# Performance work log

Measured on AMD Instinct MI355X. Metric: run time of the kernel, lower is better.

## Reference

```python
import jax, jax.numpy as jnp
from jax import lax
import numpy as np


def _conv(x, w, b):
    y = lax.conv_general_dilated(x, w, (1, 1), 'VALID', dimension_numbers=('NCHW', 'OIHW', 'NCHW'))
    return y + b[None, :, None, None]


def _prelu(x, a):
    return jnp.where(x > 0, x, a[None, :, None, None] * x)


def _pnet(x, c1w, c1b, p1, c2w, c2b, p2, c3w, c3b, p3, w41, b41, w42, b42):
    x = _prelu(_conv(x, c1w, c1b), p1)
    H, W = x.shape[2], x.shape[3]
    # MaxPool2d(2,2, ceil_mode=True): pad bottom/right with -inf when odd
    x = lax.reduce_window(x, -jnp.inf, lax.max, (1, 1, 2, 2), (1, 1, 2, 2),
                          ((0, 0), (0, 0), (0, H % 2), (0, W % 2)))
    x = _prelu(_conv(x, c2w, c2b), p2)
    x = _prelu(_conv(x, c3w, c3b), p3)
    a = jax.nn.softmax(_conv(x, w41, b41), axis=1)
    b = _conv(x, w42, b42)
    return b, a


def _nms(boxes, scores, imgidx, valid, thr):
    # masked, fixed-size batched NMS (per-image via coordinate offset trick)
    N = boxes.shape[0]
    order = jnp.argsort(-jnp.where(valid, scores, -1e9))
    b = boxes[order] + imgidx[order].astype(boxes.dtype)[:, None] * 1e5
    v = valid[order]
    x1, y1, x2, y2 = b[:, 0], b[:, 1], b[:, 2], b[:, 3]
    area = jnp.maximum(x2 - x1, 0.0) * jnp.maximum(y2 - y1, 0.0)
    ar = jnp.arange(N)

    def body(i, keep):
        iw = jnp.maximum(jnp.minimum(x2[i], x2) - jnp.maximum(x1[i], x1), 0.0)
        ih = jnp.maximum(jnp.minimum(y2[i], y2) - jnp.maximum(y1[i], y1), 0.0)
        inter = iw * ih
        iou = inter / (area[i] + area - inter + 1e-9)
        return keep & ~((iou > thr) & (ar > i) & keep[i])

    keep = lax.fori_loop(0, N, body, v)
    return order, keep


def _detect(images, c1w, c1b, p1, c2w, c2b, p2, c3w, c3b, p3, w41, b41, w42, b42):
    params = (c1w, c1b, p1, c2w, c2b, p2, c3w, c3b, p3, w41, b41, w42, b42)
    x = jnp.transpose(images, (0, 3, 1, 2))  # NHWC -> NCHW
    B, _, H, W = x.shape
    m = 12.0 / 20.0  # 12 / minsize
    scales = []
    ml, si = min(H, W) * m, m
    while ml >= 12:
        scales.append(si)
        si *= 0.709
        ml *= 0.709
    KS, THR0 = 512, 0.6  # fixed per-scale candidate capacity
    all_b, all_i, all_k = [], [], []
    for scale in scales:
        nh, nw = int(H * scale + 1), int(W * scale + 1)
        im = jax.image.resize(x, (B, 3, nh, nw), method='linear')
        im = (im - 127.5) * 0.0078125
        reg, label = _pnet(im, *params)
        probs = label[:, 1]  # [B,h,w]
        b_, h_, w_ = probs.shape
        yy, xx = jnp.meshgrid(jnp.arange(h_), jnp.arange(w_), indexing='ij')
        bbx = jnp.tile(xx.reshape(-1), b_).astype(x.dtype)
        bby = jnp.tile(yy.reshape(-1), b_).astype(x.dtype)
        # stride=2, cellsize=12 grid-cell -> image-space boxes
        q = [jnp.floor((2 * bbx + 1) / scale), jnp.floor((2 * bby + 1) / scale),
             jnp.floor((2 * bbx + 12) / scale), jnp.floor((2 * bby + 12) / scale)]
        score = probs.reshape(-1)
        reg4 = jnp.transpose(reg, (0, 2, 3, 1)).reshape(-1, 4)
        boxes9 = jnp.concatenate([jnp.stack(q + [score], axis=1), reg4], axis=1)  # [N,9]
        imgidx = jnp.repeat(jnp.arange(b_), h_ * w_)
        k = min(KS, boxes9.shape[0])
        vals, idx = lax.top_k(jnp.where(score >= THR0, score, -1e9), k)
        bsel, isel, vsel = boxes9[idx], imgidx[idx], vals > -1e8
        order, keep = _nms(bsel[:, :4], bsel[:, 4], isel, vsel, 0.5)
        all_b.append(bsel[order])
        all_i.append(isel[order])
        all_k.append(keep)
    boxes = jnp.concatenate(all_b, 0)
    iidx = jnp.concatenate(all_i, 0)
    kp = jnp.concatenate(all_k, 0)
    K2 = min(1024, boxes.shape[0])
    vals, idx = lax.top_k(jnp.where(kp, boxes[:, 4], -1e9), K2)
    b2, i2, v2 = boxes[idx], iidx[idx], vals > -1e8
    order, keep = _nms(b2[:, :4], b2[:, 4], i2, v2, 0.7)
    b2 = b2[order]
    regw, regh = b2[:, 2] - b2[:, 0], b2[:, 3] - b2[:, 1]
    out = jnp.stack([b2[:, 0] + b2[:, 5] * regw, b2[:, 1] + b2[:, 6] * regh,
                     b2[:, 2] + b2[:, 7] * regw, b2[:, 3] + b2[:, 8] * regh, b2[:, 4]], axis=1)
    # rerec: square-ify
    hh, ww = out[:, 3] - out[:, 1], out[:, 2] - out[:, 0]
    l = jnp.maximum(hh, ww)
    x1 = out[:, 0] + ww * 0.5 - l * 0.5
    y1 = out[:, 1] + hh * 0.5 - l * 0.5
    out = jnp.stack([x1, y1, x1 + l, y1 + l, out[:, 4]], axis=1)
    return out * keep[:, None].astype(out.dtype)  # invalid/suppressed rows zeroed


def setup_inputs():
    key = jax.random.key(0)
    ks = jax.random.split(key, 16)
    rn = lambda k, s, sc=0.1: jax.random.normal(k, s, dtype=jnp.float32) * sc
    return {
        'images': jax.random.uniform(ks[0], (8, 768, 768, 3), dtype=jnp.float32) * 255.0,
        'c1w': rn(ks[1], (10, 3, 3, 3)), 'c1b': rn(ks[2], (10,)),
        'p1': 0.25 * jnp.ones((10,), jnp.float32),
        'c2w': rn(ks[3], (16, 10, 3, 3)), 'c2b': rn(ks[4], (16,)),
        'p2': 0.25 * jnp.ones((16,), jnp.float32),
        'c3w': rn(ks[5], (32, 16, 3, 3)), 'c3b': rn(ks[6], (32,)),
        'p3': 0.25 * jnp.ones((32,), jnp.float32),
        'w41': rn(ks[7], (2, 32, 1, 1)), 'b41': rn(ks[8], (2,)),
        'w42': rn(ks[9], (4, 32, 1, 1)), 'b42': rn(ks[10], (4,)),
    }


def reference(images, c1w, c1b, p1, c2w, c2b, p2, c3w, c3b, p3, w41, b41, w42, b42):
    return _detect(images, c1w, c1b, p1, c2w, c2b, p2, c3w, c3b, p3, w41, b41, w42, b42)
```

## Files before the change

### kernel.cpp

```cpp
#include <hip/hip_runtime.h>
#include <stdint.h>

typedef unsigned long long u64;
typedef unsigned int u32;

#define TPB 256
#define NJMAX 12
#define NSC 11

__device__ __forceinline__ int findJob(const int* cum, int nj, int v) {
  int j = 0;
  while (j + 1 < nj && v >= cum[j + 1]) ++j;
  return j;
}

struct MkP { int ns; int nw[NSC]; float invs[NSC], ks[NSC];
             int oxB[NSC], T[NSC], wOff[NSC]; };

__global__ void k_mkweights(int* __restrict__ tX0, int* __restrict__ tCNT,
                            float* __restrict__ tWT, float* __restrict__ tW, MkP P) {
  const int s = blockIdx.x;
  const int nw = P.nw[s];
  const float invs = P.invs[s], ks = P.ks[s];
  const int T = P.T[s];
  for (int ox = threadIdx.x; ox < nw; ox += TPB) {
    float sx = ((float)ox + 0.5f) * invs - 0.5f;
    int x0 = (int)ceilf(sx - ks); if (x0 < 0) x0 = 0;
    int x1 = (int)floorf(sx + ks); if (x1 > 767) x1 = 767;
    float wt = 0.f;
    float* wv = tW + P.wOff[s];
    for (int j = x0; j <= x1; ++j) {
      float w = fmaxf(0.f, 1.f - fabsf(sx - (float)j) / ks);
      wt += w;
      wv[(j - x0) * nw + ox] = w;
    }
    for (int k = x1 - x0 + 1; k < T; ++k) wv[k * nw + ox] = 0.f;
    int g = P.oxB[s] + ox;
    tX0[g] = x0; tCNT[g] = x1 - x0 + 1; tWT[g] = wt;
  }
}

struct DscP { int nj; int N[NJMAX]; int hOff[NJMAX], imgOff[NJMAX];
              int oxB[NJMAX], wOff[NJMAX];
              int cumW[NJMAX + 1], cumR[NJMAX + 1]; };

__global__ void k_mkdesc(int* __restrict__ hd, int* __restrict__ vd,
                         int hdcap, int vdcap, DscP P) {
  int gid = blockIdx.x * TPB + threadIdx.x;
  int totW = P.cumW[P.nj], totR = P.cumR[P.nj];
  if (gid < totW) {
    int j = findJob(P.cumW, P.nj, gid);
    int local = gid - P.cumW[j];
    int N = P.N[j];
    int ox = local % N, c = local / N;
    hd[gid]             = P.hOff[j] + c * 768 * N + ox;
    hd[hdcap + gid]     = c * 769;
    hd[2 * hdcap + gid] = N;
    hd[3 * hdcap + gid] = P.oxB[j] + ox;
    hd[4 * hdcap + gid] = P.wOff[j] + ox;
  }
  if (gid < totR) {
    int j = findJob(P.cumR, P.nj, gid);
    int local = gid - P.cumR[j];
    int N = P.N[j];
    int oy = local % N, q = local / N;
    vd[gid]             = P.hOff[j] + q * 768 * N;
    vd[vdcap + gid]     = P.imgOff[j] + (q * N + oy) * N;
    vd[2 * vdcap + gid] = P.oxB[j] + oy;
    vd[3 * vdcap + gid] = P.wOff[j] + oy;
    vd[4 * vdcap + gid] = N;
  }
}

__global__ void k_resizeH_d(const float* __restrict__ img, float* __restrict__ base,
                            const int* __restrict__ tX0, const int* __restrict__ tCNT,
                            const float* __restrict__ tWT, const float* __restrict__ tW,
                            const int* __restrict__ hd, int hdcap, int total) {
  __shared__ float row[3][769];
  const int y = blockIdx.x, b = blockIdx.y;
  const float* src = img + ((long)b * 768 + y) * 768 * 3;
  for (int t = threadIdx.x; t < 2304; t += TPB) {
    int x = t / 3, c = t - 3 * x;
    row[c][x] = src[t];
  }
  __syncthreads();
  const float* rowF = &row[0][0];
  const long yb = (long)y + 2304L * b;
  for (int t = threadIdx.x; t < total; t += TPB) {
    int A = hd[t];
    int R = hd[hdcap + t];
    int N = hd[2 * hdcap + t];
    int g = hd[3 * hdcap + t];
    int W = hd[4 * hdcap + t];
    int x0 = tX0[g], cnt = tCNT[g];
    float wt = tWT[g];
    const float* wv = tW + W;
    const float* rp = rowF + R + x0;
    float acc = 0.f;
    int k = 0;
    for (; k + 3 < cnt; k += 4) {
      float v0 = rp[k],     w0 = wv[(long)k * N];
      float v1 = rp[k + 1], w1 = wv[(long)(k + 1) * N];
      float v2 = rp[k + 2], w2 = wv[(long)(k + 2) * N];
      float v3 = rp[k + 3], w3 = wv[(long)(k + 3) * N];
      acc += v0 * w0; acc += v1 * w1; acc += v2 * w2; acc += v3 * w3;
    }
    for (; k < cnt; ++k) acc += rp[k] * wv[(long)k * N];
    base[(long)A + (long)N * yb] = acc / wt;
  }
}

__global__ void k_resizeV_row(const float* __restrict__ basep, float* __restrict__ img,
                              const int* __restrict__ tX0, const int* __restrict__ tCNT,
                              const float* __restrict__ tWT, const float* __restrict__ tW,
                              const int* __restrict__ vd, int vdcap, int nRows) {
  int row = blockIdx.x * 4 + (threadIdx.x >> 6);
  if (row >= nRows) return;
  int lane = threadIdx.x & 63;
  int S = vd[row];
  int O = vd[vdcap + row];
  int g = vd[2 * vdcap + row];
  int W = vd[3 * vdcap + row];
  int N = vd[4 * vdcap + row];
  int y0 = tX0[g], cnt = tCNT[g];
  float wt = tWT[g];
  const float* wv = tW + W;
  const float* col0 = basep + S + (long)y0 * N;
  for (int ox = lane; ox < N; ox += 64) {
    const float* col = col0 + ox;
    float acc = 0.f;
    int k = 0;
    for (; k + 3 < cnt; k += 4) {
      float v0 = col[(long)k * N],       w0 = wv[(long)k * N];
      float v1 = col[(long)(k + 1) * N], w1 = wv[(long)(k + 1) * N];
      float v2 = col[(long)(k + 2) * N], w2 = wv[(long)(k + 2) * N];
      float v3 = col[(long)(k + 3) * N], w3 = wv[(long)(k + 3) * N];
      acc += v0 * w0; acc += v1 * w1; acc += v2 * w2; acc += v3 * w3;
    }
    for (; k < cnt; ++k) acc += col[(long)k * N] * wv[(long)k * N];
    img[(long)O + ox] = (acc / wt - 127.5f) * 0.0078125f;
  }
}

__device__ __forceinline__ void conv1pool_body(
    const float* in, const float* w, const float* bias, const float* pr,
    float* out, int H, int W, int co, int b, int px, int py) {
  const int h1 = H - 2, w1 = W - 2;
  const int PH = (h1 + 1) >> 1, PW = (w1 + 1) >> 1;
  if (px >= PW || py >= PH) return;
  const int x0 = px * 2, y0 = py * 2;
  float a00 = 0.f, a01 = 0.f, a10 = 0.f, a11 = 0.f;
  const float* wp = w + (long)co * 27;
  const long HW = (long)H * W;
  const float* pp = in + ((long)b * 3 * H + y0) * W + x0;
  for (int ci = 0; ci < 3; ++ci, pp += HW) {
    const float* r = pp;
    float r00 = r[0], r01 = r[1], r02 = r[2], r03 = r[3]; r += W;
    float r10 = r[0], r11 = r[1], r12 = r[2], r13 = r[3]; r += W;
    float r20 = r[0], r21 = r[1], r22 = r[2], r23 = r[3]; r += W;
    float r30 = r[0], r31 = r[1], r32 = r[2], r33 = r[3];
    const float* wc = wp + ci * 9;
    float w0 = wc[0], w1_ = wc[1], w2 = wc[2];
    float w3 = wc[3], w4 = wc[4], w5 = wc[5];
    float w6 = wc[6], w7 = wc[7], w8 = wc[8];
    a00 += r00 * w0 + r01 * w1_ + r02 * w2;
    a00 += r10 * w3 + r11 * w4 + r12 * w5;
    a00 += r20 * w6 + r21 * w7 + r22 * w8;
    a01 += r01 * w0 + r02 * w1_ + r03 * w2;
    a01 += r11 * w3 + r12 * w4 + r13 * w5;
    a01 += r21 * w6 + r22 * w7 + r23 * w8;
    a10 += r10 * w0 + r11 * w1_ + r12 * w2;
    a10 += r20 * w3 + r21 * w4 + r22 * w5;
    a10 += r30 * w6 + r31 * w7 + r32 * w8;
    a11 += r11 * w0 + r12 * w1_ + r13 * w2;
    a11 += r21 * w3 + r22 * w4 + r23 * w5;
    a11 += r31 * w6 + r32 * w7 + r33 * w8;
  }
  const float bb = bias[co], al = pr[co];
  const bool vx = (x0 + 1 < w1), vy = (y0 + 1 < h1);
  float v = a00 + bb; v = v > 0.f ? v : al * v;
  float m = v;
  if (vx) { v = a01 + bb; v = v > 0.f ? v : al * v; m = fmaxf(m, v); }
  if (vy) { v = a10 + bb; v = v > 0.f ? v : al * v; m = fmaxf(m, v); }
  if (vx && vy) { v = a11 + bb; v = v > 0.f ? v : al * v; m = fmaxf(m, v); }
  out[(((long)b * 10 + co) * PH + py) * PW + px] = m;
}

struct C1P { int nj; int nh[NJMAX]; int imgOff[NJMAX], poolOff[NJMAX];
             int t1x[NJMAX]; int cumT[NJMAX + 1]; };

__global__ void k_conv1pool_job(const float* __restrict__ imgb, const float* __restrict__ w,
                                const float* __restrict__ bias, const float* __restrict__ pr,
                                float* __restrict__ poolb, C1P P) {
  int j = findJob(P.cumT, P.nj, blockIdx.x);
  int local = blockIdx.x - P.cumT[j];
  int t1x = P.t1x[j];
  int tX = local % t1x, tY = local / t1x;
  conv1pool_body(imgb + P.imgOff[j], w, bias, pr, poolb + P.poolOff[j],
                 P.nh[j], P.nh[j], blockIdx.y, blockIdx.z,
                 tX * 16 + (threadIdx.x & 15), tY * 16 + (threadIdx.x >> 4));
}

__device__ __forceinline__ void conv3x3c8_body(
    const float* in, const float* w, const float* bias, const float* pr,
    float* out, int Cin, int Cout, int H, int W, int cog, int b, int x0, int y) {
  const int OH = H - 2, OW = W - 2;
  if (y >= OH || x0 >= OW) return;
  float acc[8][4];
#pragma unroll
  for (int k = 0; k < 8; ++k) { acc[k][0] = 0.f; acc[k][1] = 0.f; acc[k][2] = 0.f; acc[k][3] = 0.f; }
  const float* wp = w + (long)cog * Cin * 9;
  const long HW = (long)H * W;
  const float* pp = in + ((long)b * Cin * H + y) * W + x0;
  for (int ci = 0; ci < Cin; ++ci, pp += HW) {
    const float* r = pp;
    float q00 = r[0], q01 = r[1], q02 = r[2], q03 = r[3], q04 = r[4], q05 = r[5]; r += W;
    float q10 = r[0], q11 = r[1], q12 = r[2], q13 = r[3], q14 = r[4], q15 = r[5]; r += W;
    float q20 = r[0], q21 = r[1], q22 = r[2], q23 = r[3], q24 = r[4], q25 = r[5];
#pragma unroll
    for (int k = 0; k < 8; ++k) {
      const float* wc = wp + ((long)k * Cin + ci) * 9;
      float w0 = wc[0], w1 = wc[1], w2 = wc[2];
      float w3 = wc[3], w4 = wc[4], w5 = wc[5];
      float w6 = wc[6], w7 = wc[7], w8 = wc[8];
      acc[k][0] += q00 * w0 + q01 * w1 + q02 * w2;
      acc[k][1] += q01 * w0 + q02 * w1 + q03 * w2;
      acc[k][2] += q02 * w0 + q03 * w1 + q04 * w2;
      acc[k][3] += q03 * w0 + q04 * w1 + q05 * w2;
      acc[k][0] += q10 * w3 + q11 * w4 + q12 * w5;
      acc[k][1] += q11 * w3 + q12 * w4 + q13 * w5;
      acc[k][2] += q12 * w3 + q13 * w4 + q14 * w5;
      acc[k][3] += q13 * w3 + q14 * w4 + q15 * w5;
      acc[k][0] += q20 * w6 + q21 * w7 + q22 * w8;
      acc[k][1] += q21 * w6 + q22 * w7 + q23 * w8;
      acc[k][2] += q22 * w6 + q23 * w7 + q24 * w8;
      acc[k][3] += q23 * w6 + q24 * w7 + q25 * w8;
    }
  }
  const int rem = OW - x0;
#pragma unroll
  for (int k = 0; k < 8; ++k) {
    const int co = cog + k;
    const float bb = bias[co], al = pr[co];
    float* op = out + (((long)b * Cout + co) * OH + y) * OW + x0;
    float v0 = acc[k][0] + bb; v0 = v0 > 0.f ? v0 : al * v0;
    op[0] = v0;
    if (rem > 1) { float v = acc[k][1] + bb; v = v > 0.f ? v : al * v; op[1] = v; }
    if (rem > 2) { float v = acc[k][2] + bb; v = v > 0.f ? v : al * v; op[2] = v; }
    if (rem > 3) { float v = acc[k][3] + bb; v = v > 0.f ? v : al * v; op[3] = v; }
  }
}

struct CvP { int nj; int H[NJMAX]; int inOff[NJMAX], outOff[NJMAX];
             int tx[NJMAX]; int cumT[NJMAX + 1]; };

__global__ void k_conv3x3c8_job(const float* __restrict__ inb, const float* __restrict__ w,
                                const float* __restrict__ bias, const float* __restrict__ pr,
                                float* __restrict__ outb, int Cin, int Cout, CvP P) {
  int j = findJob(P.cumT, P.nj, blockIdx.x);
  int local = blockIdx.x - P.cumT[j];
  int tx0 = P.tx[j];
  int tX = local % tx0, tY = local / tx0;
  conv3x3c8_body(inb + P.inOff[j], w, bias, pr, outb + P.outOff[j], Cin, Cout,
                 P.H[j], P.H[j], blockIdx.y * 8, blockIdx.z,
                 tX * 64 + (threadIdx.x & 15) * 4, tY * 16 + (threadIdx.x >> 4));
}

__device__ __forceinline__ void head_body(const float* x3, const float* w41,
                                          const float* b41, const float* w42,
                                          const float* b42, float* reg, u64* keys,
                                          int plane, long idx) {
  int b = (int)(idx / plane); int rem = (int)(idx % plane);
  const float* p = x3 + (long)b * 32 * plane + rem;
  float l0 = 0.f, l1 = 0.f, r0 = 0.f, r1 = 0.f, r2 = 0.f, r3 = 0.f;
  for (int c = 0; c < 32; ++c) {
    float v = p[(long)c * plane];
    l0 += v * w41[c];      l1 += v * w41[32 + c];
    r0 += v * w42[c];      r1 += v * w42[32 + c];
    r2 += v * w42[64 + c]; r3 += v * w42[96 + c];
  }
  l0 += b41[0]; l1 += b41[1];
  r0 += b42[0]; r1 += b42[1]; r2 += b42[2]; r3 += b42[3];
  float mx = fmaxf(l0, l1);
  float e0 = expf(l0 - mx), e1 = expf(l1 - mx);
  float s = e1 / (e0 + e1);
  reg[idx * 4 + 0] = r0; reg[idx * 4 + 1] = r1;
  reg[idx * 4 + 2] = r2; reg[idx * 4 + 3] = r3;
  u32 ic = 0xFFFFFFFFu - (u32)idx;
  u64 k = (s >= 0.6f) ? ((((u64)__float_as_uint(s)) << 32) | ic) : (u64)ic;
  keys[idx] = k;
}

struct HdP { int nj; int h3[NJMAX]; int c3Off[NJMAX], kOff[NJMAX];
             int cumC[NJMAX + 1]; };

__global__ void k_head_job(const float* __restrict__ c3b, const float* __restrict__ w41,
                           const float* __restrict__ b41, const float* __restrict__ w42,
                           const float* __restrict__ b42, float* __restrict__ regb,
                           u64* __restrict__ keysb, HdP P) {
  int gid = blockIdx.x * TPB + threadIdx.x;
  if (gid >= P.cumC[P.nj]) return;
  int j = findJob(P.cumC, P.nj, gid);
  int idx = gid - P.cumC[j];
  head_body(c3b + P.c3Off[j], w41, b41, w42, b42,
            regb + 4L * P.kOff[j], keysb + P.kOff[j], P.h3[j] * P.h3[j], idx);
}

__device__ __forceinline__ void bitonic2048(u64* s) {
  for (int k = 2; k <= 2048; k <<= 1) {
    for (int j = k >> 1; j > 0; j >>= 1) {
      for (int i = threadIdx.x; i < 2048; i += TPB) {
        int ixj = i ^ j;
        if (ixj > i) {
          u64 a = s[i], b = s[ixj];
          bool desc = ((i & k) == 0);
          if (desc ? (a < b) : (a > b)) { s[i] = b; s[ixj] = a; }
        }
      }
      __syncthreads();
    }
  }
}

__global__ void k_topk(const u64* __restrict__ in, int n, u64* __restrict__ out, int K) {
  __shared__ u64 s[2048];
  int base = blockIdx.x * 2048;
  for (int t = threadIdx.x; t < 2048; t += TPB) {
    int gi = base + t;
    s[t] = (gi < n) ? in[gi] : 0ULL;
  }
  __syncthreads();
  bitonic2048(s);
  for (int t = threadIdx.x; t < K; t += TPB)
    out[(long)blockIdx.x * K + t] = s[t];
}

struct TkP { int nj; int srcSel[NJMAX]; int srcOff[NJMAX]; int n[NJMAX];
             int dstOff[NJMAX]; int cumB[NJMAX + 1]; };

__global__ void k_topk_job(u64* __restrict__ A, u64* __restrict__ B, TkP P) {
  __shared__ u64 s[2048];
  int j = findJob(P.cumB, P.nj, blockIdx.x);
  int lb = blockIdx.x - P.cumB[j];
  const u64* src = (P.srcSel[j] ? B : A) + P.srcOff[j];
  u64* dst = (P.srcSel[j] ? A : B) + P.dstOff[j];
  int n = P.n[j];
  int base = lb * 2048;
  for (int t = threadIdx.x; t < 2048; t += TPB) {
    int gi = base + t;
    s[t] = (gi < n) ? src[gi] : 0ULL;
  }
  __syncthreads();
  bitonic2048(s);
  for (int t = threadIdx.x; t < 512; t += TPB)
    dst[(long)lb * 512 + t] = s[t];
}

struct TkFP { int nj; int srcSel[NJMAX]; int srcOff[NJMAX]; int n[NJMAX]; int sIdx[NJMAX]; };

__global__ void k_topk_fin(const u64* __restrict__ A, const u64* __restrict__ B,
                           u64* __restrict__ selk, TkFP P) {
  __shared__ u64 s[2048];
  int j = blockIdx.x;
  const u64* src = (P.srcSel[j] ? B : A) + P.srcOff[j];
  int n = P.n[j];
  for (int t = threadIdx.x; t < 2048; t += TPB)
    s[t] = (t < n) ? src[t] : 0ULL;
  __syncthreads();
  bitonic2048(s);
  for (int t = threadIdx.x; t < 512; t += TPB)
    selk[(long)P.sIdx[j] * 512 + t] = s[t];
}

__device__ __forceinline__ void gather_body(const u64* keys, const float* reg,
                                            float* boxes, int h, int w, float scalef,
                                            int i) {
  float* bx = boxes + (long)i * 12;
  u64 key = keys[i];
  if ((key >> 32) == 0ULL) {
    for (int q = 0; q < 12; ++q) bx[q] = 0.f;
    return;
  }
  u32 cell = 0xFFFFFFFFu - (u32)(key & 0xFFFFFFFFu);
  int x = (int)(cell % (u32)w); u32 t2 = cell / (u32)w;
  int y = (int)(t2 % (u32)h); int b = (int)(t2 / (u32)h);
  float fx = (float)x, fy = (float)y;
  bx[0] = floorf((2.f * fx + 1.f) / scalef);
  bx[1] = floorf((2.f * fy + 1.f) / scalef);
  bx[2] = floorf((2.f * fx + 12.f) / scalef);
  bx[3] = floorf((2.f * fy + 12.f) / scalef);
  bx[4] = __uint_as_float((u32)(key >> 32));
  bx[5] = reg[(long)cell * 4 + 0];
  bx[6] = reg[(long)cell * 4 + 1];
  bx[7] = reg[(long)cell * 4 + 2];
  bx[8] = reg[(long)cell * 4 + 3];
  bx[9] = (float)b;
  bx[10] = 1.f;
  bx[11] = 0.f;
}

struct GtP { int nj; int h3[NJMAX]; float scalef[NJMAX]; int kOff[NJMAX]; int sIdx[NJMAX]; };

__global__ void k_gather_job(const u64* __restrict__ selk, const float* __restrict__ regb,
                             float* __restrict__ boxes, GtP P) {
  int j = blockIdx.x >> 1;
  int i = ((blockIdx.x & 1) << 8) + threadIdx.x;
  gather_body(selk + (long)P.sIdx[j] * 512, regb + 4L * P.kOff[j],
              boxes + (long)P.sIdx[j] * 512 * 12, P.h3[j], P.h3[j], P.scalef[j], i);
}

__global__ void k_nms(float* __restrict__ boxes, int per, float thr) {
  __shared__ float sx1[1024], sy1[1024], sx2[1024], sy2[1024], sar[1024];
  __shared__ unsigned char kp[1024];
  __shared__ int snv;
  float* bs = boxes + (long)blockIdx.x * per * 12;
  int N = per;
  if (threadIdx.x == 0) snv = 0;
  __syncthreads();
  for (int i = threadIdx.x; i < N; i += blockDim.x) {
    const float* b = bs + (long)i * 12;
    float off = b[9] * 100000.0f;
    float a0 = b[0] + off, a1 = b[1] + off, a2 = b[2] + off, a3 = b[3] + off;
    sx1[i] = a0; sy1[i] = a1; sx2[i] = a2; sy2[i] = a3;
    sar[i] = fmaxf(a2 - a0, 0.f) * fmaxf(a3 - a1, 0.f);
    bool v = (b[10] != 0.f);
    kp[i] = v;
    if (v) atomicMax(&snv, i + 1);
  }
  __syncthreads();
  int nv = snv;
  for (int i = 0; i < nv; ++i) {
    if (kp[i]) {
      float xi1 = sx1[i], yi1 = sy1[i], xi2 = sx2[i], yi2 = sy2[i], ai = sar[i];
      for (int j = threadIdx.x; j < nv; j += blockDim.x) {
        if (j > i && kp[j]) {
          float iw = fmaxf(fminf(xi2, sx2[j]) - fmaxf(xi1, sx1[j]), 0.f);
          float ih = fmaxf(fminf(yi2, sy2[j]) - fmaxf(yi1, sy1[j]), 0.f);
          float inter = iw * ih;
          float iou = inter / (ai + sar[j] - inter + 1e-9f);
          if (iou > thr) kp[j] = 0;
        }
      }
    }
    __syncthreads();
  }
  for (int i = threadIdx.x; i < N; i += blockDim.x)
    bs[(long)i * 12 + 11] = kp[i] ? 1.f : 0.f;
}

__global__ void k_finalkeys(const float* __restrict__ boxes, u64* __restrict__ keys,
                            int total, int padded) {
  int i = blockIdx.x * blockDim.x + threadIdx.x;
  if (i >= padded) return;
  u64 k = 0ULL;
  if (i < total) {
    const float* b = boxes + (long)i * 12;
    u32 ic = 0xFFFFFFFFu - (u32)i;
    k = (b[11] != 0.f) ? ((((u64)__float_as_uint(b[4])) << 32) | ic) : (u64)ic;
  }
  keys[i] = k;
}

__global__ void k_gatherfinal(const u64* __restrict__ keys, const float* __restrict__ boxes,
                              float* __restrict__ sel) {
  int i = blockIdx.x * blockDim.x + threadIdx.x;
  if (i >= 1024) return;
  u64 key = keys[i];
  float* o = sel + (long)i * 12;
  if ((key >> 32) == 0ULL) {
    for (int q = 0; q < 12; ++q) o[q] = 0.f;
    return;
  }
  u32 bi = 0xFFFFFFFFu - (u32)(key & 0xFFFFFFFFu);
  const float* b = boxes + (long)bi * 12;
  for (int q = 0; q < 12; ++q) o[q] = b[q];
  o[10] = 1.f;
  o[11] = 0.f;
}

__global__ void k_refine(const float* __restrict__ sel, float* __restrict__ out, int N) {
  int i = blockIdx.x * blockDim.x + threadIdx.x;
  if (i >= N) return;
  const float* b = sel + (long)i * 12;
  float keep = b[11];
  float x1 = b[0], y1 = b[1], x2 = b[2], y2 = b[3], sc = b[4];
  float rw = x2 - x1, rh = y2 - y1;
  float o0 = x1 + b[5] * rw;
  float o1 = y1 + b[6] * rh;
  float o2 = x2 + b[7] * rw;
  float o3 = y2 + b[8] * rh;
  float hh = o3 - o1, ww = o2 - o0;
  float l = fmaxf(hh, ww);
  float nx1 = o0 + ww * 0.5f - l * 0.5f;
  float ny1 = o1 + hh * 0.5f - l * 0.5f;
  out[(long)i * 5 + 0] = nx1 * keep;
  out[(long)i * 5 + 1] = ny1 * keep;
  out[(long)i * 5 + 2] = (nx1 + l) * keep;
  out[(long)i * 5 + 3] = (ny1 + l) * keep;
  out[(long)i * 5 + 4] = sc * keep;
}

extern "C" void kernel_launch(void* const* d_in, const int* in_sizes, int n_in,
                              void* d_out, int out_size, void* d_ws, size_t ws_size,
                              hipStream_t stream) {
  (void)in_sizes; (void)n_in; (void)out_size;
  const float* images = (const float*)d_in[0];
  const float* c1w = (const float*)d_in[1];
  const float* c1b = (const float*)d_in[2];
  const float* p1  = (const float*)d_in[3];
  const float* c2w = (const float*)d_in[4];
  const float* c2b = (const float*)d_in[5];
  const float* p2  = (const float*)d_in[6];
  const float* c3w = (const float*)d_in[7];
  const float* c3b = (const float*)d_in[8];
  const float* p3  = (const float*)d_in[9];
  const float* w41 = (const float*)d_in[10];
  const float* b41 = (const float*)d_in[11];
  const float* w42 = (const float*)d_in[12];
  const float* b42 = (const float*)d_in[13];
  float* ws = (float*)d_ws;

  double scl[16]; int nsc = 0;
  {
    double m = 12.0 / 20.0;
    double ml = 768.0 * m;
    double si = m;
    while (ml >= 12.0) { scl[nsc++] = si; si *= 0.709; ml *= 0.709; }
  }

  auto cdiv = [](long a, long b) { return (int)((a + b - 1) / b); };

  int NH[NSC], PH_[NSC], H2[NSC], H3[NSC], OXB[NSC], TT[NSC], WOFF[NSC];
  float INV[NSC], KSF[NSC];
  {
    int oxb = 0, woff = 0;
    for (int s = 0; s < nsc; ++s) {
      int nh = (int)(768.0 * scl[s] + 1.0);
      NH[s] = nh;
      PH_[s] = ((nh - 2) + 1) / 2;
      H2[s] = PH_[s] - 2;
      H3[s] = H2[s] - 2;
      double inv = 1.0 / (((double)nh) / 768.0);
      INV[s] = (float)inv;
      KSF[s] = (float)(inv > 1.0 ? inv : 1.0);
      TT[s] = (int)(2.0f * KSF[s]) + 2;
      OXB[s] = oxb; oxb += nh;
      WOFF[s] = woff; woff += nh * TT[s];
    }
  }

  static const int GA[11] = {0, 1, 2, 3, 4, 5, 6, 7, 8, 9, 10};
  static const int G1[7] = {0, 5, 6, 7, 8, 9, 10};
  static const int G2[4] = {1, 2, 3, 4};

  struct Layout {
    long HT, IMG, POOL, C2, REG, KEYS, SCR, SEL, BOX, FK, FS, SF, TBL, HD, VD, extent;
    int hdcap, vdcap;
  };

  auto calcLayout = [&](const int* const* gps, const int* gn, int ng,
                        int hdcap, int vdcap, Layout& L) {
    long htA = 0, c3A = 0, imgA = 0, poolA = 0, c2A = 0, cellsA = 0, scrA = 0;
    for (int g = 0; g < ng; ++g) {
      long ht = 0, c3 = 0, im = 0, pl = 0, c2s = 0, ck = 0, sc = 0;
      for (int q = 0; q < gn[g]; ++q) {
        int s = gps[g][q];
        ht += 24L * 768 * NH[s];
        im += 24L * NH[s] * NH[s];
        pl += 80L * PH_[s] * PH_[s];
        c2s += 128L * H2[s] * H2[s];
        c3 += 256L * H3[s] * H3[s];
        long cells = 8L * H3[s] * H3[s];
        ck += cells;
        sc += 512L * ((cells + 2047) / 2048);
      }
      if (ht > htA) htA = ht; if (c3 > c3A) c3A = c3; if (im > imgA) imgA = im;
      if (pl > poolA) poolA = pl; if (c2s > c2A) c2A = c2s;
      if (ck > cellsA) cellsA = ck; if (sc > scrA) scrA = sc;
    }
    long htR = htA > c3A ? htA : c3A;
    auto al = [](long v) { return (v + 15) & ~15L; };
    long off = 0;
    L.HT = off;   off += al(htR);
    L.IMG = off;  off += al(imgA);
    L.POOL = off; off += al(poolA);
    L.C2 = off;   off += al(c2A);
    L.REG = off;  off += al(4 * cellsA);
    L.KEYS = off; off += al(2 * cellsA);
    L.SCR = off;  off += al(2 * scrA + 16384);
    L.SEL = off;  off += al(11264);
    L.BOX = off;  off += al(67584);
    L.FK = off;   off += al(16384);
    L.FS = off;   off += al(2048);
    L.SF = off;   off += al(12288);
    L.TBL = off;  off += al(12288 + 24000);
    L.HD = off;   off += al((long)ng * 5 * hdcap);
    L.VD = off;   off += al((long)ng * 5 * vdcap);
    L.extent = off;
    L.hdcap = hdcap; L.vdcap = vdcap;
  };

  Layout LA, LB;
  {
    const int* gpsA[1] = {GA}; int gnA[1] = {11};
    calcLayout(gpsA, gnA, 1, 8192, 56320, LA);
    const int* gpsB[2] = {G1, G2}; int gnB[2] = {7, 4};
    calcLayout(gpsB, gnB, 2, 2560, 20480, LB);
  }
  bool big = (ws_size >= (size_t)LA.extent * 4);
  const Layout& L = big ? LA : LB;
  const int* GS[2]; int GN[2]; int ngroups;
  if (big) { GS[0] = GA; GN[0] = 11; ngroups = 1; }
  else { GS[0] = G1; GN[0] = 7; GS[1] = G2; GN[1] = 4; ngroups = 2; }

  u64* keys  = (u64*)(ws + L.KEYS);
  u64* scr   = (u64*)(ws + L.SCR);
  u64* selk  = (u64*)(ws + L.SEL);
  u64* fkeys = (u64*)(ws + L.FK);
  u64* fsel  = (u64*)(ws + L.FS);
  float* boxes = ws + L.BOX;
  float* self  = ws + L.SF;
  int*   tX0  = (int*)(ws + L.TBL);
  int*   tCNT = (int*)(ws + L.TBL + 4096);
  float* tWT  = ws + L.TBL + 8192;
  float* tW   = ws + L.TBL + 12288;

  {
    MkP P; P.ns = nsc;
    for (int s = 0; s < nsc; ++s) {
      P.nw[s] = NH[s]; P.invs[s] = INV[s]; P.ks[s] = KSF[s];
      P.oxB[s] = OXB[s]; P.T[s] = TT[s]; P.wOff[s] = WOFF[s];
    }
    k_mkweights<<<nsc, TPB, 0, stream>>>(tX0, tCNT, tWT, tW, P);
  }

  int imgOff[2][NJMAX], poolOff[2][NJMAX], c2Off[2][NJMAX], c3Off[2][NJMAX],
      htOff[2][NJMAX], kOff[2][NJMAX], cells[2][NJMAX];
  int cumWtot[2], cumRtot[2];
  for (int g = 0; g < ngroups; ++g) {
    long ch = 0, ci = 0, cp = 0, c2 = 0, c3 = 0, ck = 0;
    int cw = 0, cr = 0;
    for (int q = 0; q < GN[g]; ++q) {
      int s = GS[g][q];
      htOff[g][q] = (int)ch;  ch += 24L * 768 * NH[s];
      imgOff[g][q] = (int)ci; ci += 24L * NH[s] * NH[s];
      poolOff[g][q] = (int)cp; cp += 80L * PH_[s] * PH_[s];
      c2Off[g][q] = (int)c2;  c2 += 128L * H2[s] * H2[s];
      c3Off[g][q] = (int)c3;  c3 += 256L * H3[s] * H3[s];
      kOff[g][q] = (int)ck;   cells[g][q] = 8 * H3[s] * H3[s]; ck += cells[g][q];
      cw += 3 * NH[s]; cr += 24 * NH[s];
    }
    cumWtot[g] = cw; cumRtot[g] = cr;
  }

  for (int g = 0; g < ngroups; ++g) {
    DscP P; P.nj = GN[g];
    int cw = 0, cr = 0;
    for (int q = 0; q < GN[g]; ++q) {
      int s = GS[g][q];
      P.N[q] = NH[s]; P.hOff[q] = htOff[g][q]; P.imgOff[q] = imgOff[g][q];
      P.oxB[q] = OXB[s]; P.wOff[q] = WOFF[s];
      P.cumW[q] = cw; cw += 3 * NH[s];
      P.cumR[q] = cr; cr += 24 * NH[s];
    }
    P.cumW[GN[g]] = cw; P.cumR[GN[g]] = cr;
    int* hd = (int*)(ws + L.HD) + (long)g * 5 * L.hdcap;
    int* vd = (int*)(ws + L.VD) + (long)g * 5 * L.vdcap;
    int tot = cw > cr ? cw : cr;
    k_mkdesc<<<cdiv(tot, TPB), TPB, 0, stream>>>(hd, vd, L.hdcap, L.vdcap, P);
  }

  for (int g = 0; g < ngroups; ++g) {
    const int* gs = GS[g];
    int nj = GN[g];
    int* hd = (int*)(ws + L.HD) + (long)g * 5 * L.hdcap;
    int* vd = (int*)(ws + L.VD) + (long)g * 5 * L.vdcap;
    {
      dim3 gh(768, 8, 1);
      k_resizeH_d<<<gh, TPB, 0, stream>>>(images, ws + L.HT, tX0, tCNT, tWT, tW,
                                          hd, L.hdcap, cumWtot[g]);
    }
    k_resizeV_row<<<cdiv(cumRtot[g], 4), TPB, 0, stream>>>(
        ws + L.HT, ws + L.IMG, tX0, tCNT, tWT, tW, vd, L.vdcap, cumRtot[g]);
    {
      C1P P; P.nj = nj; int ct = 0;
      for (int q = 0; q < nj; ++q) {
        int s = gs[q];
        P.nh[q] = NH[s];
        P.imgOff[q] = imgOff[g][q]; P.poolOff[q] = poolOff[g][q];
        int t1x = cdiv(PH_[s], 16);
        P.t1x[q] = t1x;
        P.cumT[q] = ct; ct += t1x * t1x;
      }
      P.cumT[nj] = ct;
      dim3 gg(ct, 10, 8);
      k_conv1pool_job<<<gg, TPB, 0, stream>>>(ws + L.IMG, c1w, c1b, p1, ws + L.POOL, P);
    }
    {
      CvP P; P.nj = nj; int ct = 0;
      for (int q = 0; q < nj; ++q) {
        int s = gs[q];
        P.H[q] = PH_[s];
        P.inOff[q] = poolOff[g][q]; P.outOff[q] = c2Off[g][q];
        int tx = cdiv(H2[s], 64), ty = cdiv(H2[s], 16);
        P.tx[q] = tx;
        P.cumT[q] = ct; ct += tx * ty;
      }
      P.cumT[nj] = ct;
      dim3 gg(ct, 2, 8);
      k_conv3x3c8_job<<<gg, TPB, 0, stream>>>(ws + L.POOL, c2w, c2b, p2, ws + L.C2,
                                              10, 16, P);
    }
    {
      CvP P; P.nj = nj; int ct = 0;
      for (int q = 0; q < nj; ++q) {
        int s = gs[q];
        P.H[q] = H2[s];
        P.inOff[q] = c2Off[g][q]; P.outOff[q] = c3Off[g][q];
        int tx = cdiv(H3[s], 64), ty = cdiv(H3[s], 16);
        P.tx[q] = tx;
        P.cumT[q] = ct; ct += tx * ty;
      }
      P.cumT[nj] = ct;
      dim3 gg(ct, 4, 8);
      k_conv3x3c8_job<<<gg, TPB, 0, stream>>>(ws + L.C2, c3w, c3b, p3, ws + L.HT,
                                              16, 32, P);
    }
    {
      HdP P; P.nj = nj; int cc = 0;
      for (int q = 0; q < nj; ++q) {
        int s = gs[q];
        P.h3[q] = H3[s];
        P.c3Off[q] = c3Off[g][q]; P.kOff[q] = kOff[g][q];
        P.cumC[q] = cc; cc += cells[g][q];
      }
      P.cumC[nj] = cc;
      k_head_job<<<cdiv(cc, TPB), TPB, 0, stream>>>(ws + L.HT, w41, b41, w42, b42,
                                                    ws + L.REG, keys, P);
    }
    {
      int bOff[NJMAX];
      {
        int c = 0;
        for (int q = 0; q < nj; ++q) { bOff[q] = c; c += 512 * cdiv(cells[g][q], 2048); }
      }
      long nCur[NJMAX]; int par[NJMAX];
      for (int q = 0; q < nj; ++q) { nCur[q] = cells[g][q]; par[q] = 0; }
      while (true) {
        TkP P; P.nj = 0; int cum = 0; int act[NJMAX];
        for (int q = 0; q < nj; ++q) {
          if (nCur[q] > 2048) {
            int r = P.nj++;
            act[r] = q;
            int blocks = cdiv(nCur[q], 2048);
            P.srcSel[r] = par[q];
            P.srcOff[r] = par[q] ? bOff[q] : kOff[g][q];
            P.dstOff[r] = par[q] ? kOff[g][q] : bOff[q];
            P.n[r] = (int)nCur[q];
            P.cumB[r] = cum; cum += blocks;
          }
        }
        P.cumB[P.nj] = cum;
        if (P.nj == 0) break;
        k_topk_job<<<cum, TPB, 0, stream>>>(keys, scr, P);
        for (int r = 0; r < P.nj; ++r) {
          int q = act[r];
          nCur[q] = 512L * cdiv(nCur[q], 2048);
          par[q] ^= 1;
        }
      }
      TkFP F; F.nj = nj;
      for (int q = 0; q < nj; ++q) {
        F.srcSel[q] = par[q];
        F.srcOff[q] = par[q] ? bOff[q] : kOff[g][q];
        F.n[q] = (int)nCur[q];
        F.sIdx[q] = gs[q];
      }
      k_topk_fin<<<nj, TPB, 0, stream>>>(keys, scr, selk, F);
    }
    {
      GtP P; P.nj = nj;
      for (int q = 0; q < nj; ++q) {
        int s = gs[q];
        P.h3[q] = H3[s]; P.scalef[q] = (float)scl[s]; P.kOff[q] = kOff[g][q];
        P.sIdx[q] = s;
      }
      k_gather_job<<<2 * nj, TPB, 0, stream>>>(selk, ws + L.REG, boxes, P);
    }
  }

  k_nms<<<nsc, TPB, 0, stream>>>(boxes, 512, 0.5f);

  int total = nsc * 512;
  k_finalkeys<<<cdiv(8192, TPB), TPB, 0, stream>>>(boxes, fkeys, total, 8192);
  k_topk<<<4, TPB, 0, stream>>>(fkeys, 8192, scr, 1024);
  k_topk<<<2, TPB, 0, stream>>>(scr, 4096, keys, 1024);
  k_topk<<<1, TPB, 0, stream>>>(keys, 2048, fsel, 1024);
  k_gatherfinal<<<4, TPB, 0, stream>>>(fsel, boxes, self);
  k_nms<<<1, TPB, 0, stream>>>(self, 1024, 0.7f);
  k_refine<<<4, TPB, 0, stream>>>(self, (float*)d_out, 1024);
}
```

Before: 1.171 ms.

## Compute all output channels per thread in conv1 and 16 channels in conv2/3

```diff
diff --git a/kernel.cpp b/kernel.cpp
--- a/kernel.cpp
+++ b/kernel.cpp
@@ -96,16 +96,19 @@
     float wt = tWT[g];
     const float* wv = tW + W;
     const float* rp = rowF + R + x0;
+    const int N2 = N + N, N3 = N2 + N, N4 = N3 + N;
     float acc = 0.f;
     int k = 0;
+    long o = 0;
     for (; k + 3 < cnt; k += 4) {
-      float v0 = rp[k],     w0 = wv[(long)k * N];
-      float v1 = rp[k + 1], w1 = wv[(long)(k + 1) * N];
-      float v2 = rp[k + 2], w2 = wv[(long)(k + 2) * N];
-      float v3 = rp[k + 3], w3 = wv[(long)(k + 3) * N];
+      float v0 = rp[k],     w0 = wv[o];
+      float v1 = rp[k + 1], w1 = wv[o + N];
+      float v2 = rp[k + 2], w2 = wv[o + N2];
+      float v3 = rp[k + 3], w3 = wv[o + N3];
       acc += v0 * w0; acc += v1 * w1; acc += v2 * w2; acc += v3 * w3;
-    }
-    for (; k < cnt; ++k) acc += rp[k] * wv[(long)k * N];
+      o += N4;
+    }
+    for (; k < cnt; ++k) { acc += rp[k] * wv[o]; o += N; }
     base[(long)A + (long)N * yb] = acc / wt;
   }
 }
@@ -126,31 +129,35 @@
   float wt = tWT[g];
   const float* wv = tW + W;
   const float* col0 = basep + S + (long)y0 * N;
+  const int N2 = N + N, N3 = N2 + N, N4 = N3 + N;
   for (int ox = lane; ox < N; ox += 64) {
     const float* col = col0 + ox;
     float acc = 0.f;
     int k = 0;
+    long o = 0;
     for (; k + 3 < cnt; k += 4) {
-      float v0 = col[(long)k * N],       w0 = wv[(long)k * N];
-      float v1 = col[(long)(k + 1) * N], w1 = wv[(long)(k + 1) * N];
-      float v2 = col[(long)(k + 2) * N], w2 = wv[(long)(k + 2) * N];
-      float v3 = col[(long)(k + 3) * N], w3 = wv[(long)(k + 3) * N];
+      float v0 = col[o],      w0 = wv[o];
+      float v1 = col[o + N],  w1 = wv[o + N];
+      float v2 = col[o + N2], w2 = wv[o + N2];
+      float v3 = col[o + N3], w3 = wv[o + N3];
       acc += v0 * w0; acc += v1 * w1; acc += v2 * w2; acc += v3 * w3;
-    }
-    for (; k < cnt; ++k) acc += col[(long)k * N] * wv[(long)k * N];
+      o += N4;
+    }
+    for (; k < cnt; ++k) { acc += col[o] * wv[o]; o += N; }
     img[(long)O + ox] = (acc / wt - 127.5f) * 0.0078125f;
   }
 }
 
 __device__ __forceinline__ void conv1pool_body(
     const float* in, const float* w, const float* bias, const float* pr,
-    float* out, int H, int W, int co, int b, int px, int py) {
+    float* out, int H, int W, int b, int px, int py) {
   const int h1 = H - 2, w1 = W - 2;
   const int PH = (h1 + 1) >> 1, PW = (w1 + 1) >> 1;
   if (px >= PW || py >= PH) return;
   const int x0 = px * 2, y0 = py * 2;
-  float a00 = 0.f, a01 = 0.f, a10 = 0.f, a11 = 0.f;
-  const float* wp = w + (long)co * 27;
+  float a00[10], a01[10], a10[10], a11[10];
+#pragma unroll
+  for (int co = 0; co < 10; ++co) { a00[co] = 0.f; a01[co] = 0.f; a10[co] = 0.f; a11[co] = 0.f; }
   const long HW = (long)H * W;
   const float* pp = in + ((long)b * 3 * H + y0) * W + x0;
   for (int ci = 0; ci < 3; ++ci, pp += HW) {
@@ -159,31 +166,37 @@
     float r10 = r[0], r11 = r[1], r12 = r[2], r13 = r[3]; r += W;
     float r20 = r[0], r21 = r[1], r22 = r[2], r23 = r[3]; r += W;
     float r30 = r[0], r31 = r[1], r32 = r[2], r33 = r[3];
-    const float* wc = wp + ci * 9;
-    float w0 = wc[0], w1_ = wc[1], w2 = wc[2];
-    float w3 = wc[3], w4 = wc[4], w5 = wc[5];
-    float w6 = wc[6], w7 = wc[7], w8 = wc[8];
-    a00 += r00 * w0 + r01 * w1_ + r02 * w2;
-    a00 += r10 * w3 + r11 * w4 + r12 * w5;
-    a00 += r20 * w6 + r21 * w7 + r22 * w8;
-    a01 += r01 * w0 + r02 * w1_ + r03 * w2;
-    a01 += r11 * w3 + r12 * w4 + r13 * w5;
-    a01 += r21 * w6 + r22 * w7 + r23 * w8;
-    a10 += r10 * w0 + r11 * w1_ + r12 * w2;
-    a10 += r20 * w3 + r21 * w4 + r22 * w5;
-    a10 += r30 * w6 + r31 * w7 + r32 * w8;
-    a11 += r11 * w0 + r12 * w1_ + r13 * w2;
-    a11 += r21 * w3 + r22 * w4 + r23 * w5;
-    a11 += r31 * w6 + r32 * w7 + r33 * w8;
-  }
-  const float bb = bias[co], al = pr[co];
+#pragma unroll
+    for (int co = 0; co < 10; ++co) {
+      const float* wc = w + ((long)co * 3 + ci) * 9;
+      float w0 = wc[0], w1_ = wc[1], w2 = wc[2];
+      float w3 = wc[3], w4 = wc[4], w5 = wc[5];
+      float w6 = wc[6], w7 = wc[7], w8 = wc[8];
+      a00[co] += r00 * w0 + r01 * w1_ + r02 * w2;
+      a00[co] += r10 * w3 + r11 * w4 + r12 * w5;
+      a00[co] += r20 * w6 + r21 * w7 + r22 * w8;
+      a01[co] += r01 * w0 + r02 * w1_ + r03 * w2;
+      a01[co] += r11 * w3 + r12 * w4 + r13 * w5;
+      a01[co] += r21 * w6 + r22 * w7 + r23 * w8;
+      a10[co] += r10 * w0 + r11 * w1_ + r12 * w2;
+      a10[co] += r20 * w3 + r21 * w4 + r22 * w5;
+      a10[co] += r30 * w6 + r31 * w7 + r32 * w8;
+      a11[co] += r11 * w0 + r12 * w1_ + r13 * w2;
+      a11[co] += r21 * w3 + r22 * w4 + r23 * w5;
+      a11[co] += r31 * w6 + r32 * w7 + r33 * w8;
+    }
+  }
   const bool vx = (x0 + 1 < w1), vy = (y0 + 1 < h1);
-  float v = a00 + bb; v = v > 0.f ? v : al * v;
-  float m = v;
-  if (vx) { v = a01 + bb; v = v > 0.f ? v : al * v; m = fmaxf(m, v); }
-  if (vy) { v = a10 + bb; v = v > 0.f ? v : al * v; m = fmaxf(m, v); }
-  if (vx && vy) { v = a11 + bb; v = v > 0.f ? v : al * v; m = fmaxf(m, v); }
-  out[(((long)b * 10 + co) * PH + py) * PW + px] = m;
+#pragma unroll
+  for (int co = 0; co < 10; ++co) {
+    const float bb = bias[co], al = pr[co];
+    float v = a00[co] + bb; v = v > 0.f ? v : al * v;
+    float m = v;
+    if (vx) { v = a01[co] + bb; v = v > 0.f ? v : al * v; m = fmaxf(m, v); }
+    if (vy) { v = a10[co] + bb; v = v > 0.f ? v : al * v; m = fmaxf(m, v); }
+    if (vx && vy) { v = a11[co] + bb; v = v > 0.f ? v : al * v; m = fmaxf(m, v); }
+    out[(((long)b * 10 + co) * PH + py) * PW + px] = m;
+  }
 }
 
 struct C1P { int nj; int nh[NJMAX]; int imgOff[NJMAX], poolOff[NJMAX];
@@ -197,18 +210,18 @@
   int t1x = P.t1x[j];
   int tX = local % t1x, tY = local / t1x;
   conv1pool_body(imgb + P.imgOff[j], w, bias, pr, poolb + P.poolOff[j],
-                 P.nh[j], P.nh[j], blockIdx.y, blockIdx.z,
+                 P.nh[j], P.nh[j], blockIdx.z,
                  tX * 16 + (threadIdx.x & 15), tY * 16 + (threadIdx.x >> 4));
 }
 
-__device__ __forceinline__ void conv3x3c8_body(
+__device__ __forceinline__ void conv3x3c16_body(
     const float* in, const float* w, const float* bias, const float* pr,
     float* out, int Cin, int Cout, int H, int W, int cog, int b, int x0, int y) {
   const int OH = H - 2, OW = W - 2;
   if (y >= OH || x0 >= OW) return;
-  float acc[8][4];
+  float acc[16][4];
 #pragma unroll
-  for (int k = 0; k < 8; ++k) { acc[k][0] = 0.f; acc[k][1] = 0.f; acc[k][2] = 0.f; acc[k][3] = 0.f; }
+  for (int k = 0; k < 16; ++k) { acc[k][0] = 0.f; acc[k][1] = 0.f; acc[k][2] = 0.f; acc[k][3] = 0.f; }
   const float* wp = w + (long)cog * Cin * 9;
   const long HW = (long)H * W;
   const float* pp = in + ((long)b * Cin * H + y) * W + x0;
@@ -218,7 +231,7 @@
     float q10 = r[0], q11 = r[1], q12 = r[2], q13 = r[3], q14 = r[4], q15 = r[5]; r += W;
     float q20 = r[0], q21 = r[1], q22 = r[2], q23 = r[3], q24 = r[4], q25 = r[5];
 #pragma unroll
-    for (int k = 0; k < 8; ++k) {
+    for (int k = 0; k < 16; ++k) {
       const float* wc = wp + ((long)k * Cin + ci) * 9;
       float w0 = wc[0], w1 = wc[1], w2 = wc[2];
       float w3 = wc[3], w4 = wc[4], w5 = wc[5];
@@ -239,7 +252,7 @@
   }
   const int rem = OW - x0;
 #pragma unroll
-  for (int k = 0; k < 8; ++k) {
+  for (int k = 0; k < 16; ++k) {
     const int co = cog + k;
     const float bb = bias[co], al = pr[co];
     float* op = out + (((long)b * Cout + co) * OH + y) * OW + x0;
@@ -254,16 +267,16 @@
 struct CvP { int nj; int H[NJMAX]; int inOff[NJMAX], outOff[NJMAX];
              int tx[NJMAX]; int cumT[NJMAX + 1]; };
 
-__global__ void k_conv3x3c8_job(const float* __restrict__ inb, const float* __restrict__ w,
-                                const float* __restrict__ bias, const float* __restrict__ pr,
-                                float* __restrict__ outb, int Cin, int Cout, CvP P) {
+__global__ void k_conv3x3c16_job(const float* __restrict__ inb, const float* __restrict__ w,
+                                 const float* __restrict__ bias, const float* __restrict__ pr,
+                                 float* __restrict__ outb, int Cin, int Cout, CvP P) {
   int j = findJob(P.cumT, P.nj, blockIdx.x);
   int local = blockIdx.x - P.cumT[j];
   int tx0 = P.tx[j];
   int tX = local % tx0, tY = local / tx0;
-  conv3x3c8_body(inb + P.inOff[j], w, bias, pr, outb + P.outOff[j], Cin, Cout,
-                 P.H[j], P.H[j], blockIdx.y * 8, blockIdx.z,
-                 tX * 64 + (threadIdx.x & 15) * 4, tY * 16 + (threadIdx.x >> 4));
+  conv3x3c16_body(inb + P.inOff[j], w, bias, pr, outb + P.outOff[j], Cin, Cout,
+                  P.H[j], P.H[j], blockIdx.y * 16, blockIdx.z,
+                  tX * 64 + (threadIdx.x & 15) * 4, tY * 16 + (threadIdx.x >> 4));
 }
 
 __device__ __forceinline__ void head_body(const float* x3, const float* w41,
@@ -693,7 +706,7 @@
         P.cumT[q] = ct; ct += t1x * t1x;
       }
       P.cumT[nj] = ct;
-      dim3 gg(ct, 10, 8);
+      dim3 gg(ct, 1, 8);
       k_conv1pool_job<<<gg, TPB, 0, stream>>>(ws + L.IMG, c1w, c1b, p1, ws + L.POOL, P);
     }
     {
@@ -707,9 +720,9 @@
         P.cumT[q] = ct; ct += tx * ty;
       }
       P.cumT[nj] = ct;
-      dim3 gg(ct, 2, 8);
-      k_conv3x3c8_job<<<gg, TPB, 0, stream>>>(ws + L.POOL, c2w, c2b, p2, ws + L.C2,
-                                              10, 16, P);
+      dim3 gg(ct, 1, 8);
+      k_conv3x3c16_job<<<gg, TPB, 0, stream>>>(ws + L.POOL, c2w, c2b, p2, ws + L.C2,
+                                               10, 16, P);
     }
     {
       CvP P; P.nj = nj; int ct = 0;
@@ -722,9 +735,9 @@
         P.cumT[q] = ct; ct += tx * ty;
       }
       P.cumT[nj] = ct;
-      dim3 gg(ct, 4, 8);
-      k_conv3x3c8_job<<<gg, TPB, 0, stream>>>(ws + L.C2, c3w, c3b, p3, ws + L.HT,
-                                              16, 32, P);
+      dim3 gg(ct, 2, 8);
+      k_conv3x3c16_job<<<gg, TPB, 0, stream>>>(ws + L.C2, c3w, c3b, p3, ws + L.HT,
+                                               16, 32, P);
     }
     {
       HdP P; P.nj = nj; int cc = 0;
```

After: 1.283 ms. 1.1x slower.
